# Kernel optimization log

Measured on AMD Instinct MI355X. Metric: run time of the kernel, lower is better.

The kernel has to match this reference:

```python
import jax, jax.numpy as jnp
import numpy as np
from jax import lax


def _leaky(x):
    # LeakyReLU, negative_slope=0.1
    return jnp.where(x > 0, x, 0.1 * x)


def _conv(x, w, pad, groups=1):
    # NCHW / OIHW 2D conv, stride 1
    return lax.conv_general_dilated(
        x, w, (1, 1), [(pad, pad), (pad, pad)],
        dimension_numbers=("NCHW", "OIHW", "NCHW"),
        feature_group_count=groups)


def setup_inputs() -> dict:
    key = jax.random.key(0)
    ks = jax.random.split(key, 12)
    B, C, H, W = 16, 64, 256, 256
    KS = 3

    def nrm(k, shape, fan_in):
        return jax.random.normal(k, shape, jnp.float32) / np.float32(np.sqrt(fan_in))

    return {
        "x": jax.random.normal(ks[0], (B, C, H, W), jnp.float32),
        "t": jax.random.normal(ks[1], (B, 1, 1, 1), jnp.float32),
        # t_process: 1x1 convs (1->64, 64->64), no bias -> stored as matrices
        "tW1": nrm(ks[2], (C, 1), 1),
        "tW2": nrm(ks[3], (C, C), C),
        # f_process: two 3x3 convs 64->64 with bias
        "fW1": nrm(ks[4], (C, C, KS, KS), C * KS * KS),
        "fb1": jnp.zeros((C,), jnp.float32),
        "fW2": nrm(ks[5], (C, C, KS, KS), C * KS * KS),
        "fb2": jnp.zeros((C,), jnp.float32),
        # kernel branch: 1x1 convs (1->64, 64->64*9), no bias
        "kW1": nrm(ks[6], (C, 1), 1),
        "kW2": nrm(ks[7], (C * KS * KS, C), C),
        # conv33: 3x3 conv 64->64 with bias
        "cW": nrm(ks[8], (C, C, KS, KS), C * KS * KS),
        "cb": jnp.zeros((C,), jnp.float32),
    }


def reference(x, t, tW1, tW2, fW1, fb1, fW2, fb2, kW1, kW2, cW, cb):
    b, c, h, w = x.shape
    KS = 3

    # f_process: Conv3x3 -> LeakyReLU -> Conv3x3 -> LeakyReLU
    f = _leaky(_conv(x, fW1, 1) + fb1[None, :, None, None])
    f = _leaky(_conv(f, fW2, 1) + fb2[None, :, None, None])

    # t is (b,1,1,1); 1x1 convs on it are per-sample matmuls
    ts = t.reshape(b, 1)
    # t_process: Conv1x1 -> LeakyReLU -> Conv1x1 -> Sigmoid -> (b,c,1,1)
    mv = jax.nn.sigmoid(_leaky(ts @ tW1.T) @ tW2.T).reshape(b, c, 1, 1)

    # kernel branch: Conv1x1 -> LeakyReLU -> Conv1x1 -> LeakyReLU -> (b*c,1,3,3)
    kern = _leaky(_leaky(ts @ kW1.T) @ kW2.T).reshape(b * c, 1, KS, KS)

    # per-sample-channel dynamic depthwise conv: groups = b*c
    out = _conv(f.reshape(1, b * c, h, w), kern, (KS - 1) // 2,
                groups=b * c).reshape(b, c, h, w)

    # modulation gating + residual 3x3 conv
    return out * mv + _conv(x, cW, 1) + cb[None, :, None, None]
```

## Files before the change

kernel.cpp:

```cpp
#include <hip/hip_runtime.h>
#include <cstdint>

using short8  = __attribute__((ext_vector_type(8))) short;
using short4v = __attribute__((ext_vector_type(4))) short;
using f32x16  = __attribute__((ext_vector_type(16))) float;
using float4v = __attribute__((ext_vector_type(4))) float;
typedef unsigned short ushort_t;

__device__ __forceinline__ float lrelu(float x) { return x > 0.f ? x : 0.1f * x; }

__device__ __forceinline__ ushort_t f2bf(float f) {
    union { float f; unsigned u; } v; v.f = f;
    unsigned r = (v.u + 0x7FFFu + ((v.u >> 16) & 1u)) >> 16;
    return (ushort_t)r;
}
__device__ __forceinline__ float bf2f(ushort_t b) {
    union { unsigned u; float f; } v; v.u = ((unsigned)b) << 16; return v.f;
}

__device__ __forceinline__ void gload_lds16(const ushort_t* g, ushort_t* l) {
    __builtin_amdgcn_global_load_lds(
        (const __attribute__((address_space(1))) void*)g,
        (__attribute__((address_space(3))) void*)l, 16, 0, 0);
}

__global__ void k_tiny(const float* __restrict__ t, const float* __restrict__ tW1,
                       const float* __restrict__ tW2, const float* __restrict__ kW1,
                       const float* __restrict__ kW2, float* __restrict__ ktr) {
    int b = blockIdx.x;
    int c = threadIdx.x;
    __shared__ float h1[64], g1[64];
    float ts = t[b];
    h1[c] = lrelu(ts * tW1[c]);
    g1[c] = lrelu(ts * kW1[c]);
    __syncthreads();
    float s = 0.f;
    for (int j = 0; j < 64; ++j) s = fmaf(tW2[c * 64 + j], h1[j], s);
    float mvv = 1.f / (1.f + expf(-s));
    for (int q = 0; q < 9; ++q) {
        float s2 = 0.f;
        for (int j = 0; j < 64; ++j) s2 = fmaf(kW2[(c * 9 + q) * 64 + j], g1[j], s2);
        ktr[b * 576 + q * 64 + c] = lrelu(s2) * mvv;
    }
}

__global__ void k_zrow(ushort_t* __restrict__ z) {
    int i = blockIdx.x * 256 + threadIdx.x;
    *(short8*)(z + (size_t)i * 8) = (short8)0;
}

__global__ void k_pack(const float* __restrict__ w1, const float* __restrict__ w2,
                       const float* __restrict__ w3, ushort_t* __restrict__ wp) {
    int idx = blockIdx.x * 256 + threadIdx.x;
    if (idx >= 3 * 36864) return;
    int conv = idx / 36864, r = idx % 36864;
    const float* W = conv == 0 ? w1 : (conv == 1 ? w2 : w3);
    int j = r & 7, lane = (r >> 3) & 63, ct = (r >> 9) & 1, kc = (r >> 10) & 1,
        ch = (r >> 11) & 1, t = r >> 12;
    int co = ct * 32 + (lane & 31);
    int ci = ch * 32 + kc * 16 + (lane >> 5) * 8 + j;
    wp[idx] = f2bf(W[(co * 64 + ci) * 9 + t]);
}

__global__ __launch_bounds__(256) void k_tr(const float* __restrict__ x,
                                            ushort_t* __restrict__ xbf) {
    int bid = blockIdx.x;
    int h = bid & 255, b = bid >> 8;
    int t = threadIdx.x;
    for (int it = 0; it < 8; ++it) {
        int idx = t + it * 256;
        int g = idx & 7, w = idx >> 3;
        const float* src = x + (((size_t)(b * 64 + g * 8) * 256 + h) * 256 + w);
        short8 v;
#pragma unroll
        for (int j = 0; j < 8; ++j) v[j] = (short)f2bf(src[(size_t)j * 65536]);
        *(short8*)(xbf + (((size_t)(b * 256 + h) * 256 + w) * 64 + g * 8)) = v;
    }
}

__global__ __launch_bounds__(256, 3) void k_conv13(
    const ushort_t* __restrict__ in, const ushort_t* __restrict__ zv,
    const ushort_t* __restrict__ wpa, const ushort_t* __restrict__ wpc,
    const float* __restrict__ ba, const float* __restrict__ bc,
    ushort_t* __restrict__ f1out, float* __restrict__ cres) {
    __shared__ __align__(16) ushort_t xs[3136 * 8];
    const int tid = threadIdx.x;
    const int lane = tid & 63;
    const int wv = tid >> 6;
    const unsigned bid = blockIdx.x;
    const unsigned L = (bid & 7u) * 512u + (bid >> 3);
    const int h = L & 255, b = L >> 8;
    const int l31 = lane & 31, lhi = lane >> 5;
    const int pw0 = wv * 64;

    const ushort_t* rb0 = (h > 0)   ? in + ((size_t)(b * 256 + h - 1)) * 16384 : zv;
    const ushort_t* rb1 =             in + ((size_t)(b * 256 + h)) * 16384;
    const ushort_t* rb2 = (h < 255) ? in + ((size_t)(b * 256 + h + 1)) * 16384 : zv;

    f32x16 accA[2][2], accC[2][2];
#pragma unroll
    for (int a = 0; a < 2; ++a)
#pragma unroll
        for (int c = 0; c < 2; ++c) { accA[a][c] = (f32x16)0.0f; accC[a][c] = (f32x16)0.0f; }

    for (int ch = 0; ch < 2; ++ch) {
        __syncthreads();
#pragma unroll
        for (int it = 0; it < 13; ++it) {
            int base = it * 256 + wv * 64;
            if (base < 3120) {
                int S = base + lane;
                S = S < 3120 ? S : 3119;
                int r = (S >= 2080) ? 2 : (S >= 1040 ? 1 : 0);
                int rem = S - r * 1040;
                int m = rem >> 3, sl = rem & 7;
                int sp = sl ^ (m & 7);
                int p = 2 * m + (sp >> 2), g = sp & 3;
                int ws = p - 1;
                bool edge = (unsigned)ws >= 256u;
                const ushort_t* rp = (r == 0) ? rb0 : (r == 1 ? rb1 : rb2);
                const ushort_t* src = edge ? zv : (rp + ws * 64 + ch * 32 + g * 8);
                gload_lds16(src, xs + (size_t)base * 8);
            }
        }
        asm volatile("s_waitcnt vmcnt(0)" ::: "memory");
        __syncthreads();

#pragma unroll
        for (int t = 0; t < 9; ++t) {
            const int dw = t % 3;
            const int rr = t / 3;
#pragma unroll
            for (int kc = 0; kc < 2; ++kc) {
                const int off = ((((t * 2 + ch) * 2 + kc) * 2) * 64 + lane) * 8;
                short8 a0 = *(const short8*)(wpa + off);
                short8 a1 = *(const short8*)(wpa + off + 512);
                short8 c0 = *(const short8*)(wpc + off);
                short8 c1 = *(const short8*)(wpc + off + 512);
                const int g = kc * 2 + lhi;
#pragma unroll
                for (int pt = 0; pt < 2; ++pt) {
                    int p = pw0 + pt * 32 + l31 + dw;
                    int slot = ((p & 1) * 4 + g) ^ ((p >> 1) & 7);
                    short8 bf = *(const short8*)(xs + (((size_t)rr * 130 + (p >> 1)) * 8 + slot) * 8);
                    accA[0][pt] = __builtin_amdgcn_mfma_f32_32x32x16_bf16(a0, bf, accA[0][pt], 0, 0, 0);
                    accA[1][pt] = __builtin_amdgcn_mfma_f32_32x32x16_bf16(a1, bf, accA[1][pt], 0, 0, 0);
                    accC[0][pt] = __builtin_amdgcn_mfma_f32_32x32x16_bf16(c0, bf, accC[0][pt], 0, 0, 0);
                    accC[1][pt] = __builtin_amdgcn_mfma_f32_32x32x16_bf16(c1, bf, accC[1][pt], 0, 0, 0);
                }
            }
        }
    }

    const int co_b = 4 * lhi;
    {
        ushort_t* outb = f1out + ((size_t)(b * 256 + h)) * 16384;
#pragma unroll
        for (int ct = 0; ct < 2; ++ct)
#pragma unroll
            for (int pt = 0; pt < 2; ++pt) {
                int pix = pw0 + pt * 32 + l31;
                ushort_t* po = outb + (size_t)pix * 64 + ct * 32 + co_b;
#pragma unroll
                for (int q = 0; q < 4; ++q) {
                    float4v bv = *(const float4v*)(ba + ct * 32 + co_b + 8 * q);
                    short4v sv;
#pragma unroll
                    for (int m = 0; m < 4; ++m) {
                        float v = lrelu(accA[ct][pt][q * 4 + m] + bv[m]);
                        sv[m] = (short)f2bf(v);
                    }
                    *(short4v*)(po + 8 * q) = sv;
                }
            }
    }
    {
        float* pb = cres + (((size_t)b * 64) << 16) + h * 256;
#pragma unroll
        for (int ct = 0; ct < 2; ++ct)
#pragma unroll
            for (int pt = 0; pt < 2; ++pt) {
                int pix = pw0 + pt * 32 + l31;
#pragma unroll
                for (int q = 0; q < 4; ++q) {
                    float4v bv = *(const float4v*)(bc + ct * 32 + co_b + 8 * q);
#pragma unroll
                    for (int m = 0; m < 4; ++m) {
                        int c = ct * 32 + co_b + 8 * q + m;
                        pb[((size_t)c << 16) + pix] = accC[ct][pt][q * 4 + m] + bv[m];
                    }
                }
            }
    }
}

__global__ __launch_bounds__(256, 3) void k_conv2(const ushort_t* __restrict__ in,
                                                  const ushort_t* __restrict__ zv,
                                                  const ushort_t* __restrict__ wp,
                                                  const float* __restrict__ bias,
                                                  ushort_t* __restrict__ outp) {
    __shared__ __align__(16) ushort_t xs[3136 * 8];
    const int tid = threadIdx.x;
    const int lane = tid & 63;
    const int wv = tid >> 6;
    const unsigned bid = blockIdx.x;
    const unsigned L = (bid & 7u) * 512u + (bid >> 3);
    const int h = L & 255, b = L >> 8;
    const int l31 = lane & 31, lhi = lane >> 5;
    const int pw0 = wv * 64;

    const ushort_t* rb0 = (h > 0)   ? in + ((size_t)(b * 256 + h - 1)) * 16384 : zv;
    const ushort_t* rb1 =             in + ((size_t)(b * 256 + h)) * 16384;
    const ushort_t* rb2 = (h < 255) ? in + ((size_t)(b * 256 + h + 1)) * 16384 : zv;

    f32x16 acc[2][2];
#pragma unroll
    for (int a = 0; a < 2; ++a)
#pragma unroll
        for (int c = 0; c < 2; ++c) acc[a][c] = (f32x16)0.0f;

    for (int ch = 0; ch < 2; ++ch) {
        __syncthreads();
#pragma unroll
        for (int it = 0; it < 13; ++it) {
            int base = it * 256 + wv * 64;
            if (base < 3120) {
                int S = base + lane;
                S = S < 3120 ? S : 3119;
                int r = (S >= 2080) ? 2 : (S >= 1040 ? 1 : 0);
                int rem = S - r * 1040;
                int m = rem >> 3, sl = rem & 7;
                int sp = sl ^ (m & 7);
                int p = 2 * m + (sp >> 2), g = sp & 3;
                int ws = p - 1;
                bool edge = (unsigned)ws >= 256u;
                const ushort_t* rp = (r == 0) ? rb0 : (r == 1 ? rb1 : rb2);
                const ushort_t* src = edge ? zv : (rp + ws * 64 + ch * 32 + g * 8);
                gload_lds16(src, xs + (size_t)base * 8);
            }
        }
        asm volatile("s_waitcnt vmcnt(0)" ::: "memory");
        __syncthreads();

#pragma unroll
        for (int t = 0; t < 9; ++t) {
            const int dw = t % 3;
            const int rr = t / 3;
#pragma unroll
            for (int kc = 0; kc < 2; ++kc) {
                const ushort_t* wpf = wp + (((((t * 2 + ch) * 2 + kc) * 2) * 64 + lane) * 8);
                short8 a0 = *(const short8*)(wpf);
                short8 a1 = *(const short8*)(wpf + 512);
                const int g = kc * 2 + lhi;
#pragma unroll
                for (int pt = 0; pt < 2; ++pt) {
                    int p = pw0 + pt * 32 + l31 + dw;
                    int slot = ((p & 1) * 4 + g) ^ ((p >> 1) & 7);
                    short8 bf = *(const short8*)(xs + (((size_t)rr * 130 + (p >> 1)) * 8 + slot) * 8);
                    acc[0][pt] = __builtin_amdgcn_mfma_f32_32x32x16_bf16(a0, bf, acc[0][pt], 0, 0, 0);
                    acc[1][pt] = __builtin_amdgcn_mfma_f32_32x32x16_bf16(a1, bf, acc[1][pt], 0, 0, 0);
                }
            }
        }
    }

    const int co_b = 4 * lhi;
    ushort_t* pb = outp + (((size_t)b * 64) << 16) + h * 256;
#pragma unroll
    for (int ct = 0; ct < 2; ++ct)
#pragma unroll
        for (int pt = 0; pt < 2; ++pt) {
            int pix = pw0 + pt * 32 + l31;
#pragma unroll
            for (int q = 0; q < 4; ++q) {
                float4v bv = *(const float4v*)(bias + ct * 32 + co_b + 8 * q);
#pragma unroll
                for (int m = 0; m < 4; ++m) {
                    int c = ct * 32 + co_b + 8 * q + m;
                    float v = lrelu(acc[ct][pt][q * 4 + m] + bv[m]);
                    pb[((size_t)c << 16) + pix] = f2bf(v);
                }
            }
        }
}

__global__ __launch_bounds__(256) void k_fin(const ushort_t* __restrict__ f2,
                                             const float* __restrict__ ktr,
                                             float* __restrict__ out) {
    __shared__ __align__(16) ushort_t s[10 * 272];
    const unsigned bid = blockIdx.x;
    const unsigned L = (bid & 7u) * 4096u + (bid >> 3);
    const int hb = L & 31, c = (L >> 5) & 63, b = L >> 11;
    const int h0 = hb * 8;
    const int w = threadIdx.x;

    const ushort_t* f2c = f2 + (((size_t)(b * 64 + c)) << 16);
    for (int i = w; i < 320; i += 256) {
        int r = i >> 5, seg = i & 31;
        int hs = h0 - 1 + r;
        short8 v = (short8)0;
        if ((unsigned)hs < 256u) v = *(const short8*)(f2c + hs * 256 + seg * 8);
        *(short8*)(&s[r * 272 + 8 + seg * 8]) = v;
        if (seg == 0) s[r * 272 + 7] = 0;
        if (seg == 31) s[r * 272 + 264] = 0;
    }
    __syncthreads();

    float kv[9];
#pragma unroll
    for (int t9 = 0; t9 < 9; ++t9) kv[t9] = ktr[b * 576 + t9 * 64 + c];

    float lv[10], cv[10], rv[10];
#pragma unroll
    for (int r = 0; r < 10; ++r) {
        lv[r] = bf2f(s[r * 272 + 7 + w]);
        cv[r] = bf2f(s[r * 272 + 8 + w]);
        rv[r] = bf2f(s[r * 272 + 9 + w]);
    }

    float* ob = out + (((size_t)(b * 64 + c)) << 16) + h0 * 256 + w;
#pragma unroll
    for (int rr = 0; rr < 8; ++rr) {
        float dwv = 0.f;
#pragma unroll
        for (int r3 = 0; r3 < 3; ++r3) {
            dwv = fmaf(kv[r3 * 3 + 0], lv[rr + r3], dwv);
            dwv = fmaf(kv[r3 * 3 + 1], cv[rr + r3], dwv);
            dwv = fmaf(kv[r3 * 3 + 2], rv[rr + r3], dwv);
        }
        float* po = ob + rr * 256;
        *po = *po + dwv;
    }
}

extern "C" void kernel_launch(void* const* d_in, const int* in_sizes, int n_in,
                              void* d_out, int out_size, void* d_ws, size_t ws_size,
                              hipStream_t stream) {
    const float* x   = (const float*)d_in[0];
    const float* t   = (const float*)d_in[1];
    const float* tW1 = (const float*)d_in[2];
    const float* tW2 = (const float*)d_in[3];
    const float* fW1 = (const float*)d_in[4];
    const float* fb1 = (const float*)d_in[5];
    const float* fW2 = (const float*)d_in[6];
    const float* fb2 = (const float*)d_in[7];
    const float* kW1 = (const float*)d_in[8];
    const float* kW2 = (const float*)d_in[9];
    const float* cW  = (const float*)d_in[10];
    const float* cb  = (const float*)d_in[11];

    char* ws = (char*)d_ws;
    float*    ktr  = (float*)ws;
    ushort_t* wp   = (ushort_t*)(ws + 65536);
    ushort_t* zv   = (ushort_t*)(ws + 294912);
    ushort_t* xbf  = (ushort_t*)(ws + (512u << 10));
    ushort_t* f1bf = (ushort_t*)(ws + (512u << 10) + ((size_t)128 << 20));
    ushort_t* f2n  = xbf;
    float*    out  = (float*)d_out;

    k_tiny<<<dim3(16), dim3(64), 0, stream>>>(t, tW1, tW2, kW1, kW2, ktr);
    k_zrow<<<dim3(8), dim3(256), 0, stream>>>(zv);
    k_pack<<<dim3((3 * 36864 + 255) / 256), dim3(256), 0, stream>>>(fW1, fW2, cW, wp);
    k_tr<<<dim3(4096), dim3(256), 0, stream>>>(x, xbf);

    k_conv13<<<dim3(4096), dim3(256), 0, stream>>>(
        xbf, zv, wp, wp + 2 * 36864, fb1, cb, f1bf, out);
    k_conv2<<<dim3(4096), dim3(256), 0, stream>>>(f1bf, zv, wp + 36864, fb2, f2n);
    k_fin<<<dim3(32768), dim3(256), 0, stream>>>(f2n, ktr, out);
}
```

Measured before the change: 716.1 us.

## Double-buffer LDS staging over four 16-channel chunks in both conv kernels

Splits the 64 input channels into four 16-channel chunks and stages them into two alternating LDS buffers with async global-to-LDS loads. Each chunk's MFMA work now overlaps the load of the next chunk, instead of loading half the channels and then computing behind a full barrier. The weight packing layout and the LDS swizzle are changed to match the new chunk order. MFMA sections raise wave priority with s_setprio. The fused conv kernel's launch bound is lowered from 3 to 2 blocks per CU, which may reduce occupancy.

```diff
diff --git a/kernel.cpp b/kernel.cpp
--- a/kernel.cpp
+++ b/kernel.cpp
@@ -6,6 +6,11 @@
 using f32x16  = __attribute__((ext_vector_type(16))) float;
 using float4v = __attribute__((ext_vector_type(4))) float;
 typedef unsigned short ushort_t;
+
+#define CHUNK_ROW 520
+#define CHUNK_SLOTS 1560
+#define BUF_SLOTS 1632
+#define BUF_SHORTS (BUF_SLOTS * 8)
 
 __device__ __forceinline__ float lrelu(float x) { return x > 0.f ? x : 0.1f * x; }
 
@@ -55,10 +60,10 @@
     if (idx >= 3 * 36864) return;
     int conv = idx / 36864, r = idx % 36864;
     const float* W = conv == 0 ? w1 : (conv == 1 ? w2 : w3);
-    int j = r & 7, lane = (r >> 3) & 63, ct = (r >> 9) & 1, kc = (r >> 10) & 1,
-        ch = (r >> 11) & 1, t = r >> 12;
+    int j = r & 7, lane = (r >> 3) & 63, ct = (r >> 9) & 1, chunk = (r >> 10) & 3,
+        t = r >> 12;
     int co = ct * 32 + (lane & 31);
-    int ci = ch * 32 + kc * 16 + (lane >> 5) * 8 + j;
+    int ci = chunk * 16 + (lane >> 5) * 8 + j;
     wp[idx] = f2bf(W[(co * 64 + ci) * 9 + t]);
 }
 
@@ -78,12 +83,36 @@
     }
 }
 
-__global__ __launch_bounds__(256, 3) void k_conv13(
+#define STAGE_CHUNK(chunk, bufbase)                                              \
+    {                                                                            \
+        _Pragma("unroll")                                                        \
+        for (int i_ = 0; i_ < 7; ++i_) {                                         \
+            int base_ = wv * 390 + i_ * 64;                                      \
+            int S_ = base_ + lane;                                               \
+            S_ = S_ < CHUNK_SLOTS ? S_ : CHUNK_SLOTS - 1;                        \
+            int row_ = (S_ >= 2 * CHUNK_ROW) ? 2 : (S_ >= CHUNK_ROW ? 1 : 0);    \
+            int rem_ = S_ - row_ * CHUNK_ROW;                                    \
+            int mg_ = rem_ >> 3, sl_ = rem_ & 7;                                 \
+            int sp_ = sl_ ^ (mg_ & 7);                                           \
+            int p_ = mg_ * 4 + (sp_ >> 1), g_ = sp_ & 1;                         \
+            int wsx_ = p_ - 1;                                                   \
+            bool edge_ = (unsigned)wsx_ >= 256u;                                 \
+            const ushort_t* rp_ = (row_ == 0) ? rb0 : (row_ == 1 ? rb1 : rb2);   \
+            const ushort_t* src_ =                                               \
+                edge_ ? zv : (rp_ + wsx_ * 64 + (chunk)*16 + g_ * 8);            \
+            gload_lds16(src_, xs + (bufbase) + (size_t)base_ * 8);               \
+        }                                                                        \
+    }
+
+#define VMCNT(n) asm volatile("s_waitcnt vmcnt(" #n ")" ::: "memory")
+#define RBAR() __builtin_amdgcn_s_barrier()
+
+__global__ __launch_bounds__(256, 2) void k_conv13(
     const ushort_t* __restrict__ in, const ushort_t* __restrict__ zv,
     const ushort_t* __restrict__ wpa, const ushort_t* __restrict__ wpc,
     const float* __restrict__ ba, const float* __restrict__ bc,
     ushort_t* __restrict__ f1out, float* __restrict__ cres) {
-    __shared__ __align__(16) ushort_t xs[3136 * 8];
+    __shared__ __align__(16) ushort_t xs[2 * BUF_SHORTS];
     const int tid = threadIdx.x;
     const int lane = tid & 63;
     const int wv = tid >> 6;
@@ -103,54 +132,52 @@
 #pragma unroll
         for (int c = 0; c < 2; ++c) { accA[a][c] = (f32x16)0.0f; accC[a][c] = (f32x16)0.0f; }
 
-    for (int ch = 0; ch < 2; ++ch) {
-        __syncthreads();
-#pragma unroll
-        for (int it = 0; it < 13; ++it) {
-            int base = it * 256 + wv * 64;
-            if (base < 3120) {
-                int S = base + lane;
-                S = S < 3120 ? S : 3119;
-                int r = (S >= 2080) ? 2 : (S >= 1040 ? 1 : 0);
-                int rem = S - r * 1040;
-                int m = rem >> 3, sl = rem & 7;
-                int sp = sl ^ (m & 7);
-                int p = 2 * m + (sp >> 2), g = sp & 3;
-                int ws = p - 1;
-                bool edge = (unsigned)ws >= 256u;
-                const ushort_t* rp = (r == 0) ? rb0 : (r == 1 ? rb1 : rb2);
-                const ushort_t* src = edge ? zv : (rp + ws * 64 + ch * 32 + g * 8);
-                gload_lds16(src, xs + (size_t)base * 8);
-            }
-        }
-        asm volatile("s_waitcnt vmcnt(0)" ::: "memory");
-        __syncthreads();
-
-#pragma unroll
-        for (int t = 0; t < 9; ++t) {
-            const int dw = t % 3;
-            const int rr = t / 3;
-#pragma unroll
-            for (int kc = 0; kc < 2; ++kc) {
-                const int off = ((((t * 2 + ch) * 2 + kc) * 2) * 64 + lane) * 8;
-                short8 a0 = *(const short8*)(wpa + off);
-                short8 a1 = *(const short8*)(wpa + off + 512);
-                short8 c0 = *(const short8*)(wpc + off);
-                short8 c1 = *(const short8*)(wpc + off + 512);
-                const int g = kc * 2 + lhi;
-#pragma unroll
-                for (int pt = 0; pt < 2; ++pt) {
-                    int p = pw0 + pt * 32 + l31 + dw;
-                    int slot = ((p & 1) * 4 + g) ^ ((p >> 1) & 7);
-                    short8 bf = *(const short8*)(xs + (((size_t)rr * 130 + (p >> 1)) * 8 + slot) * 8);
-                    accA[0][pt] = __builtin_amdgcn_mfma_f32_32x32x16_bf16(a0, bf, accA[0][pt], 0, 0, 0);
-                    accA[1][pt] = __builtin_amdgcn_mfma_f32_32x32x16_bf16(a1, bf, accA[1][pt], 0, 0, 0);
-                    accC[0][pt] = __builtin_amdgcn_mfma_f32_32x32x16_bf16(c0, bf, accC[0][pt], 0, 0, 0);
-                    accC[1][pt] = __builtin_amdgcn_mfma_f32_32x32x16_bf16(c1, bf, accC[1][pt], 0, 0, 0);
-                }
-            }
-        }
-    }
+#define COMPUTE13(chunk, bufbase)                                                   \
+    {                                                                               \
+        __builtin_amdgcn_s_setprio(1);                                              \
+        _Pragma("unroll")                                                           \
+        for (int t_ = 0; t_ < 9; ++t_) {                                            \
+            const int dwx_ = t_ % 3, rr_ = t_ / 3;                                  \
+            const int off_ = ((t_ * 4 + (chunk)) * 2) * 512 + lane * 8;             \
+            short8 a0 = *(const short8*)(wpa + off_);                               \
+            short8 a1 = *(const short8*)(wpa + off_ + 512);                         \
+            short8 c0 = *(const short8*)(wpc + off_);                               \
+            short8 c1 = *(const short8*)(wpc + off_ + 512);                         \
+            _Pragma("unroll")                                                       \
+            for (int pt_ = 0; pt_ < 2; ++pt_) {                                     \
+                int p_ = pw0 + pt_ * 32 + l31 + dwx_;                               \
+                int mg_ = p_ >> 2;                                                  \
+                int sl_ = ((p_ & 3) * 2 + lhi) ^ (mg_ & 7);                         \
+                short8 bf = *(const short8*)(                                       \
+                    xs + (bufbase) + (size_t)(rr_ * CHUNK_ROW + mg_ * 8 + sl_) * 8);\
+                accA[0][pt_] = __builtin_amdgcn_mfma_f32_32x32x16_bf16(a0, bf, accA[0][pt_], 0, 0, 0); \
+                accA[1][pt_] = __builtin_amdgcn_mfma_f32_32x32x16_bf16(a1, bf, accA[1][pt_], 0, 0, 0); \
+                accC[0][pt_] = __builtin_amdgcn_mfma_f32_32x32x16_bf16(c0, bf, accC[0][pt_], 0, 0, 0); \
+                accC[1][pt_] = __builtin_amdgcn_mfma_f32_32x32x16_bf16(c1, bf, accC[1][pt_], 0, 0, 0); \
+            }                                                                       \
+        }                                                                           \
+        __builtin_amdgcn_s_setprio(0);                                              \
+    }
+
+    STAGE_CHUNK(0, 0);
+    STAGE_CHUNK(1, BUF_SHORTS);
+    VMCNT(7);
+    RBAR();
+    COMPUTE13(0, 0);
+    RBAR();
+    STAGE_CHUNK(2, 0);
+    VMCNT(7);
+    RBAR();
+    COMPUTE13(1, BUF_SHORTS);
+    RBAR();
+    STAGE_CHUNK(3, BUF_SHORTS);
+    VMCNT(7);
+    RBAR();
+    COMPUTE13(2, 0);
+    RBAR();
+    VMCNT(0);
+    RBAR();
+    COMPUTE13(3, BUF_SHORTS);
 
     const int co_b = 4 * lhi;
     {
@@ -192,6 +219,7 @@
                 }
             }
     }
+#undef COMPUTE13
 }
 
 __global__ __launch_bounds__(256, 3) void k_conv2(const ushort_t* __restrict__ in,
@@ -199,7 +227,7 @@
                                                   const ushort_t* __restrict__ wp,
                                                   const float* __restrict__ bias,
                                                   ushort_t* __restrict__ outp) {
-    __shared__ __align__(16) ushort_t xs[3136 * 8];
+    __shared__ __align__(16) ushort_t xs[2 * BUF_SHORTS];
     const int tid = threadIdx.x;
     const int lane = tid & 63;
     const int wv = tid >> 6;
@@ -219,50 +247,48 @@
 #pragma unroll
         for (int c = 0; c < 2; ++c) acc[a][c] = (f32x16)0.0f;
 
-    for (int ch = 0; ch < 2; ++ch) {
-        __syncthreads();
-#pragma unroll
-        for (int it = 0; it < 13; ++it) {
-            int base = it * 256 + wv * 64;
-            if (base < 3120) {
-                int S = base + lane;
-                S = S < 3120 ? S : 3119;
-                int r = (S >= 2080) ? 2 : (S >= 1040 ? 1 : 0);
-                int rem = S - r * 1040;
-                int m = rem >> 3, sl = rem & 7;
-                int sp = sl ^ (m & 7);
-                int p = 2 * m + (sp >> 2), g = sp & 3;
-                int ws = p - 1;
-                bool edge = (unsigned)ws >= 256u;
-                const ushort_t* rp = (r == 0) ? rb0 : (r == 1 ? rb1 : rb2);
-                const ushort_t* src = edge ? zv : (rp + ws * 64 + ch * 32 + g * 8);
-                gload_lds16(src, xs + (size_t)base * 8);
-            }
-        }
-        asm volatile("s_waitcnt vmcnt(0)" ::: "memory");
-        __syncthreads();
-
-#pragma unroll
-        for (int t = 0; t < 9; ++t) {
-            const int dw = t % 3;
-            const int rr = t / 3;
-#pragma unroll
-            for (int kc = 0; kc < 2; ++kc) {
-                const ushort_t* wpf = wp + (((((t * 2 + ch) * 2 + kc) * 2) * 64 + lane) * 8);
-                short8 a0 = *(const short8*)(wpf);
-                short8 a1 = *(const short8*)(wpf + 512);
-                const int g = kc * 2 + lhi;
-#pragma unroll
-                for (int pt = 0; pt < 2; ++pt) {
-                    int p = pw0 + pt * 32 + l31 + dw;
-                    int slot = ((p & 1) * 4 + g) ^ ((p >> 1) & 7);
-                    short8 bf = *(const short8*)(xs + (((size_t)rr * 130 + (p >> 1)) * 8 + slot) * 8);
-                    acc[0][pt] = __builtin_amdgcn_mfma_f32_32x32x16_bf16(a0, bf, acc[0][pt], 0, 0, 0);
-                    acc[1][pt] = __builtin_amdgcn_mfma_f32_32x32x16_bf16(a1, bf, acc[1][pt], 0, 0, 0);
-                }
-            }
-        }
-    }
+#define COMPUTE2(chunk, bufbase)                                                    \
+    {                                                                               \
+        __builtin_amdgcn_s_setprio(1);                                              \
+        _Pragma("unroll")                                                           \
+        for (int t_ = 0; t_ < 9; ++t_) {                                            \
+            const int dwx_ = t_ % 3, rr_ = t_ / 3;                                  \
+            const int off_ = ((t_ * 4 + (chunk)) * 2) * 512 + lane * 8;             \
+            short8 a0 = *(const short8*)(wp + off_);                                \
+            short8 a1 = *(const short8*)(wp + off_ + 512);                          \
+            _Pragma("unroll")                                                       \
+            for (int pt_ = 0; pt_ < 2; ++pt_) {                                     \
+                int p_ = pw0 + pt_ * 32 + l31 + dwx_;                               \
+                int mg_ = p_ >> 2;                                                  \
+                int sl_ = ((p_ & 3) * 2 + lhi) ^ (mg_ & 7);                         \
+                short8 bf = *(const short8*)(                                       \
+                    xs + (bufbase) + (size_t)(rr_ * CHUNK_ROW + mg_ * 8 + sl_) * 8);\
+                acc[0][pt_] = __builtin_amdgcn_mfma_f32_32x32x16_bf16(a0, bf, acc[0][pt_], 0, 0, 0); \
+                acc[1][pt_] = __builtin_amdgcn_mfma_f32_32x32x16_bf16(a1, bf, acc[1][pt_], 0, 0, 0); \
+            }                                                                       \
+        }                                                                           \
+        __builtin_amdgcn_s_setprio(0);                                              \
+    }
+
+    STAGE_CHUNK(0, 0);
+    STAGE_CHUNK(1, BUF_SHORTS);
+    VMCNT(7);
+    RBAR();
+    COMPUTE2(0, 0);
+    RBAR();
+    STAGE_CHUNK(2, 0);
+    VMCNT(7);
+    RBAR();
+    COMPUTE2(1, BUF_SHORTS);
+    RBAR();
+    STAGE_CHUNK(3, BUF_SHORTS);
+    VMCNT(7);
+    RBAR();
+    COMPUTE2(2, 0);
+    RBAR();
+    VMCNT(0);
+    RBAR();
+    COMPUTE2(3, BUF_SHORTS);
 
     const int co_b = 4 * lhi;
     ushort_t* pb = outp + (((size_t)b * 64) << 16) + h * 256;
@@ -282,6 +308,7 @@
                 }
             }
         }
+#undef COMPUTE2
 }
 
 __global__ __launch_bounds__(256) void k_fin(const ushort_t* __restrict__ f2,
```

After: 631.1 us. 1.13x faster.
